# Optimization experiments

Measured on AMD Instinct MI355X. Metric: run time of the kernel, lower is better.

The kernel has to match this reference:

```python
import jax, jax.numpy as jnp
import numpy as np

K = 3        # kernel_size
UM = 2       # um_dim
EPS = 1e-6
SLOPE = 0.01 # F.leaky_relu default negative slope


def setup_inputs() -> dict:
    key = jax.random.key(0)
    k1, k2, k3 = jax.random.split(key, 3)
    B, C, H, Wd = 16, 64, 64, 64
    O = 64
    xx = jax.random.normal(k1, (B, C, H, Wd), dtype=jnp.float32)
    W = jax.random.normal(k2, (O, C, K, K), dtype=jnp.float32) * 0.05
    b = jax.random.normal(k3, (O,), dtype=jnp.float32) * 0.05
    return {"xx": xx, "W": W, "b": b}


def reference(xx, W, b):
    B, C, H, Wd = xx.shape
    O = W.shape[0]
    p = (K - 1) // 2
    # replicate pad (mode='replicate' in torch == 'edge' in numpy/jax)
    xp = jnp.pad(xx, ((0, 0), (0, 0), (p, p), (p, p)), mode='edge')
    # unfold -> patches[b, c, i, j, h, w] = xp[b, c, h+i, w+j]; stride==1
    pats = jnp.stack(
        [xp[:, :, i:i + H, j:j + Wd] for i in range(K) for j in range(K)],
        axis=2,
    ).reshape(B, C, K, K, H, Wd)
    # min-max "std" normalization over (channel-group, ki, kj)
    g = pats.reshape(B, C // UM, UM, K, K, H, Wd)
    stds = (g.max(axis=(1, 3, 4), keepdims=True)
            - g.min(axis=(1, 3, 4), keepdims=True))  # [B,1,UM,1,1,H,W]
    normed = (g / (stds + EPS)).reshape(B, C, K, K, H, Wd)
    # patch-conv with stride=k on the unfolded image is equivalent to this
    # per-position contraction; big[b,c,h*k+j, w*k+i] = normed[b,c,i,j,h,w]
    # so the kernel indexes as W[o, c, j, i].
    out = jnp.einsum('bcijhw,ocji->bohw', normed, W) + b[None, :, None, None]
    out = jnp.where(out >= 0, out, SLOPE * out)  # leaky_relu
    # inverse transform: re-scale by (stds + eps)
    stds_s = stds.reshape(B, 1, UM, H, Wd)
    out = out.reshape(B, O // UM, UM, H, Wd) * (stds_s + EPS)
    return out.reshape(B, O, H, Wd)
```

## Files before the change

kernel.cpp:

```cpp
#include <hip/hip_runtime.h>
#include <hip/hip_bf16.h>

#define B_  16
#define C_  64
#define H_  64
#define W_  64
#define O_  64
#define EPS 1e-6f
#define SLOPE 0.01f

typedef __bf16  bf16x8 __attribute__((ext_vector_type(8)));
typedef float   f32x4  __attribute__((ext_vector_type(4)));

#define XT_OFF   0
#define XT_SZ    36864
#define PMIN_OFF 36864
#define PMAX_OFF 38912
#define SINV_OFF 40960
#define SEPS_OFF 42000
#undef  SEPS_OFF
#define SEPS_OFF 41984
#define SMEM_SZ  43008

__device__ __forceinline__ unsigned short f2bf(float f) {
  unsigned u = __float_as_uint(f);
  u += 0x7fffu + ((u >> 16) & 1u);
  return (unsigned short)(u >> 16);
}

__device__ __forceinline__ int clampi(int v, int lo, int hi) {
  return v < lo ? lo : (v > hi ? hi : v);
}

__global__ void wtransform_kernel(const float* __restrict__ Wsrc,
                                  unsigned short* __restrict__ Wt) {
  int idx = blockIdx.x * 256 + threadIdx.x;
  if (idx >= O_ * C_ * 9) return;
  int i = idx % 3;
  int j = (idx / 3) % 3;
  int c = (idx / 9) % C_;
  int o = idx / (9 * C_);
  int tap = i * 3 + j;
  Wt[((tap * 2 + (c & 1)) * 64 + o) * 32 + (c >> 1)] = f2bf(Wsrc[idx]);
}

__launch_bounds__(256, 3)
__global__ void conv_main_kernel(const float* __restrict__ x,
                                 const unsigned short* __restrict__ Wt,
                                 const float* __restrict__ bias,
                                 float* __restrict__ out) {
  __shared__ char smem[SMEM_SZ];
  const int tid  = threadIdx.x;
  const int lane = tid & 63;
  const int wv   = tid >> 6;
  const int b    = blockIdx.x >> 5;
  const int h0   = (blockIdx.x & 31) << 1;

  {
    const int w = tid & 63;
    const int r = tid >> 6;
    const int hr = clampi(h0 - 1 + r, 0, H_ - 1);
    const float* xb = x + ((size_t)b * C_ * H_ * W_) + hr * W_ + w;
    float mn[2] = {3.4e38f, 3.4e38f}, mx[2] = {-3.4e38f, -3.4e38f};
    #pragma unroll
    for (int pm = 0; pm < 8; ++pm) {
      const int p = pm >> 2, m = pm & 3;
      unsigned d[4];
      #pragma unroll
      for (int e = 0; e < 4; ++e) {
        const int c2a = m * 8 + 2 * e;
        const float f0 = xb[(2 * c2a + p) * (H_ * W_)];
        const float f1 = xb[(2 * (c2a + 1) + p) * (H_ * W_)];
        mn[p] = fminf(mn[p], fminf(f0, f1));
        mx[p] = fmaxf(mx[p], fmaxf(f0, f1));
        d[e] = (unsigned)f2bf(f0) | ((unsigned)f2bf(f1) << 16);
      }
      *(uint4*)(smem + XT_OFF + (r * 64 + w) * 144 + p * 64 + m * 16) =
          make_uint4(d[0], d[1], d[2], d[3]);
    }
    ((float*)(smem + PMIN_OFF))[(0 * 4 + r) * 64 + w] = mn[0];
    ((float*)(smem + PMIN_OFF))[(1 * 4 + r) * 64 + w] = mn[1];
    ((float*)(smem + PMAX_OFF))[(0 * 4 + r) * 64 + w] = mx[0];
    ((float*)(smem + PMAX_OFF))[(1 * 4 + r) * 64 + w] = mx[1];
  }
  __syncthreads();

  {
    const int hh = tid >> 7, p = (tid >> 6) & 1, w = tid & 63;
    const float* pmin = (const float*)(smem + PMIN_OFF);
    const float* pmax = (const float*)(smem + PMAX_OFF);
    float mn = 3.4e38f, mx = -3.4e38f;
    #pragma unroll
    for (int r = 0; r < 3; ++r) {
      #pragma unroll
      for (int dw = -1; dw <= 1; ++dw) {
        const int wc = clampi(w + dw, 0, W_ - 1);
        mn = fminf(mn, pmin[(p * 4 + (hh + r)) * 64 + wc]);
        mx = fmaxf(mx, pmax[(p * 4 + (hh + r)) * 64 + wc]);
      }
    }
    const float sv = (mx - mn) + EPS;
    ((float*)(smem + SEPS_OFF))[(hh * 2 + p) * 64 + w] = sv;
    ((float*)(smem + SINV_OFF))[(hh * 2 + p) * 64 + w] = 1.0f / sv;
  }
  __syncthreads();

  const int o0  = wv * 16;
  const int l15 = lane & 15;
  const int q   = lane >> 4;

  const f32x4 zero = {0.0f, 0.0f, 0.0f, 0.0f};
  f32x4 acc[2][2][4];
  #pragma unroll
  for (int p = 0; p < 2; ++p)
    #pragma unroll
    for (int hh = 0; hh < 2; ++hh)
      #pragma unroll
      for (int nt = 0; nt < 4; ++nt) acc[p][hh][nt] = zero;

  #pragma unroll
  for (int p = 0; p < 2; ++p) {
    bf16x8 af[9];
    #pragma unroll
    for (int t9 = 0; t9 < 9; ++t9)
      af[t9] = *(const bf16x8*)(Wt + ((t9 * 2 + p) * 64 + o0 + l15) * 32 + q * 8);
    #pragma unroll
    for (int xr = 0; xr < 4; ++xr) {
      #pragma unroll
      for (int nt = 0; nt < 4; ++nt) {
        bf16x8 bfr[3];
        #pragma unroll
        for (int j = 0; j < 3; ++j) {
          const int wc = clampi(nt * 16 + l15 + j - 1, 0, W_ - 1);
          bfr[j] = *(const bf16x8*)(smem + XT_OFF + (xr * 64 + wc) * 144 + p * 64 + q * 16);
        }
        #pragma unroll
        for (int hh = 0; hh < 2; ++hh) {
          const int i = xr - hh;
          if (i >= 0 && i < 3) {
            #pragma unroll
            for (int j = 0; j < 3; ++j)
              acc[p][hh][nt] = __builtin_amdgcn_mfma_f32_16x16x32_bf16(
                  af[i * 3 + j], bfr[j], acc[p][hh][nt], 0, 0, 0);
          }
        }
      }
    }
  }

  const float* sinv = (const float*)(smem + SINV_OFF);
  const float* seps = (const float*)(smem + SEPS_OFF);
  #pragma unroll
  for (int hh = 0; hh < 2; ++hh) {
    #pragma unroll
    for (int nt = 0; nt < 4; ++nt) {
      const int wpx = nt * 16 + l15;
      const float s0 = sinv[(hh * 2 + 0) * 64 + wpx];
      const float s1 = sinv[(hh * 2 + 1) * 64 + wpx];
      const float se0 = seps[(hh * 2 + 0) * 64 + wpx];
      const float se1 = seps[(hh * 2 + 1) * 64 + wpx];
      #pragma unroll
      for (int reg = 0; reg < 4; ++reg) {
        const int o = o0 + q * 4 + reg;
        float v = acc[0][hh][nt][reg] * s0 + acc[1][hh][nt][reg] * s1 + bias[o];
        v = v >= 0.0f ? v : SLOPE * v;
        v *= (o & 1) ? se1 : se0;
        out[((b * O_ + o) * H_ + (h0 + hh)) * W_ + wpx] = v;
      }
    }
  }
}

extern "C" void kernel_launch(void* const* d_in, const int* in_sizes, int n_in,
                              void* d_out, int out_size, void* d_ws, size_t ws_size,
                              hipStream_t stream) {
  const float* x    = (const float*)d_in[0];
  const float* Wsrc = (const float*)d_in[1];
  const float* bias = (const float*)d_in[2];
  float* out = (float*)d_out;
  unsigned short* Wt = (unsigned short*)d_ws;

  wtransform_kernel<<<144, 256, 0, stream>>>(Wsrc, Wt);
  conv_main_kernel<<<512, 256, 0, stream>>>(x, Wt, bias, out);
}
```

Baseline: 81.94 us.

## Double threads per block, split output rows across waves, swizzle block order

The conv kernel moves to 512 threads per block, with each wave owning one output row and 16 output channels. This removes the redundant per-wave loop over both rows and halves the accumulator registers. The staging load is split across two channel halves, so per-pixel min/max partials are combined from two sets. Weight fragments are loaded before the first barrier to overlap with staging, blocks are remapped so that concurrently scheduled blocks touch different batches, and the transformed weights move from the workspace to a device global. The cost is a larger block with a barrier-heavy prologue that uses only half the threads in the stats stage.

```diff
diff --git a/kernel.cpp b/kernel.cpp
--- a/kernel.cpp
+++ b/kernel.cpp
@@ -14,13 +14,13 @@
 
 #define XT_OFF   0
 #define XT_SZ    36864
-#define PMIN_OFF 36864
-#define PMAX_OFF 38912
-#define SINV_OFF 40960
-#define SEPS_OFF 42000
-#undef  SEPS_OFF
-#define SEPS_OFF 41984
-#define SMEM_SZ  43008
+#define PMIN_OFF (XT_OFF + XT_SZ)
+#define PMAX_OFF (PMIN_OFF + 4096)
+#define SINV_OFF (PMAX_OFF + 4096)
+#define SEPS_OFF (SINV_OFF + 1024)
+#define SMEM_SZ  (SEPS_OFF + 1024)
+
+__device__ __align__(16) unsigned short g_Wt[O_ * C_ * 9];
 
 __device__ __forceinline__ unsigned short f2bf(float f) {
   unsigned u = __float_as_uint(f);
@@ -32,8 +32,7 @@
   return v < lo ? lo : (v > hi ? hi : v);
 }
 
-__global__ void wtransform_kernel(const float* __restrict__ Wsrc,
-                                  unsigned short* __restrict__ Wt) {
+__global__ void wtransform_kernel(const float* __restrict__ Wsrc) {
   int idx = blockIdx.x * 256 + threadIdx.x;
   if (idx >= O_ * C_ * 9) return;
   int i = idx % 3;
@@ -41,52 +40,66 @@
   int c = (idx / 9) % C_;
   int o = idx / (9 * C_);
   int tap = i * 3 + j;
-  Wt[((tap * 2 + (c & 1)) * 64 + o) * 32 + (c >> 1)] = f2bf(Wsrc[idx]);
+  g_Wt[((tap * 2 + (c & 1)) * 64 + o) * 32 + (c >> 1)] = f2bf(Wsrc[idx]);
 }
 
-__launch_bounds__(256, 3)
+__launch_bounds__(512, 4)
 __global__ void conv_main_kernel(const float* __restrict__ x,
-                                 const unsigned short* __restrict__ Wt,
                                  const float* __restrict__ bias,
                                  float* __restrict__ out) {
-  __shared__ char smem[SMEM_SZ];
+  __shared__ __align__(16) char smem[SMEM_SZ];
   const int tid  = threadIdx.x;
   const int lane = tid & 63;
   const int wv   = tid >> 6;
-  const int b    = blockIdx.x >> 5;
-  const int h0   = (blockIdx.x & 31) << 1;
+
+  const int bid  = (int)blockIdx.x;
+  const int obid = (bid & 7) * 64 + (bid >> 3);
+  const int b    = obid >> 5;
+  const int h0   = (obid & 31) << 1;
 
   {
-    const int w = tid & 63;
-    const int r = tid >> 6;
+    const int w    = tid & 63;
+    const int r    = (tid >> 6) & 3;
+    const int half = tid >> 8;
     const int hr = clampi(h0 - 1 + r, 0, H_ - 1);
     const float* xb = x + ((size_t)b * C_ * H_ * W_) + hr * W_ + w;
     float mn[2] = {3.4e38f, 3.4e38f}, mx[2] = {-3.4e38f, -3.4e38f};
     #pragma unroll
-    for (int pm = 0; pm < 8; ++pm) {
-      const int p = pm >> 2, m = pm & 3;
+    for (int pm = 0; pm < 4; ++pm) {
+      const int p = pm >> 1, m = pm & 1;
       unsigned d[4];
       #pragma unroll
       for (int e = 0; e < 4; ++e) {
-        const int c2a = m * 8 + 2 * e;
+        const int c2a = half * 16 + m * 8 + 2 * e;
         const float f0 = xb[(2 * c2a + p) * (H_ * W_)];
         const float f1 = xb[(2 * (c2a + 1) + p) * (H_ * W_)];
         mn[p] = fminf(mn[p], fminf(f0, f1));
         mx[p] = fmaxf(mx[p], fmaxf(f0, f1));
         d[e] = (unsigned)f2bf(f0) | ((unsigned)f2bf(f1) << 16);
       }
-      *(uint4*)(smem + XT_OFF + (r * 64 + w) * 144 + p * 64 + m * 16) =
+      *(uint4*)(smem + XT_OFF + (r * 64 + w) * 144 + p * 64 + half * 32 + m * 16) =
           make_uint4(d[0], d[1], d[2], d[3]);
     }
-    ((float*)(smem + PMIN_OFF))[(0 * 4 + r) * 64 + w] = mn[0];
-    ((float*)(smem + PMIN_OFF))[(1 * 4 + r) * 64 + w] = mn[1];
-    ((float*)(smem + PMAX_OFF))[(0 * 4 + r) * 64 + w] = mx[0];
-    ((float*)(smem + PMAX_OFF))[(1 * 4 + r) * 64 + w] = mx[1];
+    ((float*)(smem + PMIN_OFF))[((half * 2 + 0) * 4 + r) * 64 + w] = mn[0];
+    ((float*)(smem + PMIN_OFF))[((half * 2 + 1) * 4 + r) * 64 + w] = mn[1];
+    ((float*)(smem + PMAX_OFF))[((half * 2 + 0) * 4 + r) * 64 + w] = mx[0];
+    ((float*)(smem + PMAX_OFF))[((half * 2 + 1) * 4 + r) * 64 + w] = mx[1];
   }
+
+  const int l15 = lane & 15;
+  const int q   = lane >> 4;
+  const int hh  = wv >> 2;
+  const int o0  = (wv & 3) << 4;
+
+  bf16x8 af[9];
+  #pragma unroll
+  for (int t9 = 0; t9 < 9; ++t9)
+    af[t9] = *(const bf16x8*)(g_Wt + ((t9 * 2 + 0) * 64 + o0 + l15) * 32 + q * 8);
+
   __syncthreads();
 
-  {
-    const int hh = tid >> 7, p = (tid >> 6) & 1, w = tid & 63;
+  if (tid < 256) {
+    const int shh = tid >> 7, sp = (tid >> 6) & 1, sw = tid & 63;
     const float* pmin = (const float*)(smem + PMIN_OFF);
     const float* pmax = (const float*)(smem + PMAX_OFF);
     float mn = 3.4e38f, mx = -3.4e38f;
@@ -94,56 +107,48 @@
     for (int r = 0; r < 3; ++r) {
       #pragma unroll
       for (int dw = -1; dw <= 1; ++dw) {
-        const int wc = clampi(w + dw, 0, W_ - 1);
-        mn = fminf(mn, pmin[(p * 4 + (hh + r)) * 64 + wc]);
-        mx = fmaxf(mx, pmax[(p * 4 + (hh + r)) * 64 + wc]);
+        const int wc = clampi(sw + dw, 0, W_ - 1);
+        mn = fminf(mn, fminf(pmin[((0 * 2 + sp) * 4 + shh + r) * 64 + wc],
+                             pmin[((1 * 2 + sp) * 4 + shh + r) * 64 + wc]));
+        mx = fmaxf(mx, fmaxf(pmax[((0 * 2 + sp) * 4 + shh + r) * 64 + wc],
+                             pmax[((1 * 2 + sp) * 4 + shh + r) * 64 + wc]));
       }
     }
     const float sv = (mx - mn) + EPS;
-    ((float*)(smem + SEPS_OFF))[(hh * 2 + p) * 64 + w] = sv;
-    ((float*)(smem + SINV_OFF))[(hh * 2 + p) * 64 + w] = 1.0f / sv;
+    ((float*)(smem + SEPS_OFF))[(shh * 2 + sp) * 64 + sw] = sv;
+    ((float*)(smem + SINV_OFF))[(shh * 2 + sp) * 64 + sw] = 1.0f / sv;
   }
   __syncthreads();
 
-  const int o0  = wv * 16;
-  const int l15 = lane & 15;
-  const int q   = lane >> 4;
-
   const f32x4 zero = {0.0f, 0.0f, 0.0f, 0.0f};
-  f32x4 acc[2][2][4];
+  f32x4 acc[2][4];
   #pragma unroll
   for (int p = 0; p < 2; ++p)
     #pragma unroll
-    for (int hh = 0; hh < 2; ++hh)
-      #pragma unroll
-      for (int nt = 0; nt < 4; ++nt) acc[p][hh][nt] = zero;
+    for (int nt = 0; nt < 4; ++nt) acc[p][nt] = zero;
 
   #pragma unroll
   for (int p = 0; p < 2; ++p) {
-    bf16x8 af[9];
+    if (p == 1) {
+      #pragma unroll
+      for (int t9 = 0; t9 < 9; ++t9)
+        af[t9] = *(const bf16x8*)(g_Wt + ((t9 * 2 + 1) * 64 + o0 + l15) * 32 + q * 8);
+    }
     #pragma unroll
-    for (int t9 = 0; t9 < 9; ++t9)
-      af[t9] = *(const bf16x8*)(Wt + ((t9 * 2 + p) * 64 + o0 + l15) * 32 + q * 8);
-    #pragma unroll
-    for (int xr = 0; xr < 4; ++xr) {
+    for (int ri = 0; ri < 3; ++ri) {
+      const int r = hh + ri;
       #pragma unroll
       for (int nt = 0; nt < 4; ++nt) {
         bf16x8 bfr[3];
         #pragma unroll
         for (int j = 0; j < 3; ++j) {
           const int wc = clampi(nt * 16 + l15 + j - 1, 0, W_ - 1);
-          bfr[j] = *(const bf16x8*)(smem + XT_OFF + (xr * 64 + wc) * 144 + p * 64 + q * 16);
+          bfr[j] = *(const bf16x8*)(smem + XT_OFF + (r * 64 + wc) * 144 + p * 64 + q * 16);
         }
         #pragma unroll
-        for (int hh = 0; hh < 2; ++hh) {
-          const int i = xr - hh;
-          if (i >= 0 && i < 3) {
-            #pragma unroll
-            for (int j = 0; j < 3; ++j)
-              acc[p][hh][nt] = __builtin_amdgcn_mfma_f32_16x16x32_bf16(
-                  af[i * 3 + j], bfr[j], acc[p][hh][nt], 0, 0, 0);
-          }
-        }
+        for (int j = 0; j < 3; ++j)
+          acc[p][nt] = __builtin_amdgcn_mfma_f32_16x16x32_bf16(
+              af[ri * 3 + j], bfr[j], acc[p][nt], 0, 0, 0);
       }
     }
   }
@@ -151,22 +156,19 @@
   const float* sinv = (const float*)(smem + SINV_OFF);
   const float* seps = (const float*)(smem + SEPS_OFF);
   #pragma unroll
-  for (int hh = 0; hh < 2; ++hh) {
+  for (int nt = 0; nt < 4; ++nt) {
+    const int wpx = nt * 16 + l15;
+    const float s0  = sinv[(hh * 2 + 0) * 64 + wpx];
+    const float s1  = sinv[(hh * 2 + 1) * 64 + wpx];
+    const float se0 = seps[(hh * 2 + 0) * 64 + wpx];
+    const float se1 = seps[(hh * 2 + 1) * 64 + wpx];
     #pragma unroll
-    for (int nt = 0; nt < 4; ++nt) {
-      const int wpx = nt * 16 + l15;
-      const float s0 = sinv[(hh * 2 + 0) * 64 + wpx];
-      const float s1 = sinv[(hh * 2 + 1) * 64 + wpx];
-      const float se0 = seps[(hh * 2 + 0) * 64 + wpx];
-      const float se1 = seps[(hh * 2 + 1) * 64 + wpx];
-      #pragma unroll
-      for (int reg = 0; reg < 4; ++reg) {
-        const int o = o0 + q * 4 + reg;
-        float v = acc[0][hh][nt][reg] * s0 + acc[1][hh][nt][reg] * s1 + bias[o];
-        v = v >= 0.0f ? v : SLOPE * v;
-        v *= (o & 1) ? se1 : se0;
-        out[((b * O_ + o) * H_ + (h0 + hh)) * W_ + wpx] = v;
-      }
+    for (int reg = 0; reg < 4; ++reg) {
+      const int o = o0 + q * 4 + reg;
+      float v = acc[0][nt][reg] * s0 + acc[1][nt][reg] * s1 + bias[o];
+      v = v >= 0.0f ? v : SLOPE * v;
+      v *= (o & 1) ? se1 : se0;
+      out[((b * O_ + o) * H_ + (h0 + hh)) * W_ + wpx] = v;
     }
   }
 }
@@ -178,8 +180,8 @@
   const float* Wsrc = (const float*)d_in[1];
   const float* bias = (const float*)d_in[2];
   float* out = (float*)d_out;
-  unsigned short* Wt = (unsigned short*)d_ws;
+  (void)d_ws; (void)ws_size;
 
-  wtransform_kernel<<<144, 256, 0, stream>>>(Wsrc, Wt);
-  conv_main_kernel<<<512, 256, 0, stream>>>(x, Wt, bias, out);
+  wtransform_kernel<<<144, 256, 0, stream>>>(Wsrc);
+  conv_main_kernel<<<512, 512, 0, stream>>>(x, bias, out);
 }
```

Result: no change. 83.38 us (+1.8%).
